# Kernel tuning notes

Measured on AMD Instinct MI355X. Metric: run time of the kernel, lower is better.

The kernel has to match this reference:

```python
import jax, jax.numpy as jnp
import numpy as np

DELTA = 0.1
NEG_INF = -1e30


def setup_inputs() -> dict:
    key = jax.random.key(0)
    k1, k2, k3, k4 = jax.random.split(key, 4)
    Bs, Bt, D, C = 8192, 8192, 64, 10
    return {
        "src_feas": jax.random.normal(k1, (Bs, D), dtype=jnp.float32),
        "src_labels": jax.random.randint(k2, (Bs,), 0, C, dtype=jnp.int32),
        "tgt_feas": jax.random.normal(k3, (Bt, D), dtype=jnp.float32),
        "tgt_logits": jax.random.normal(k4, (Bt, C), dtype=jnp.float32),
    }


def reference(src_feas, src_labels, tgt_feas, tgt_logits):
    # The original builds the explicit list of positive pairs (i_tgt, j_src)
    # where tgt sample i is 'confident' (top1-top2 logit gap >= delta) and
    # src_labels[j] == argmax(tgt_logits[i]).  The [P, P] score matrix it
    # forms is s[k, l] = src_feas[j_k] . tgt_feas[i_l], which only depends on
    # (j_k, i_l), so sum(diag(log_softmax(s))) collapses to a weighted
    # logsumexp over the [Bs, Bt] cross-domain score matrix. Same math,
    # fully vectorized, order-invariant.
    Bs = src_feas.shape[0]
    C = tgt_logits.shape[1]

    top2 = jax.lax.top_k(tgt_logits, 2)[0]                  # [Bt, 2]
    conf = (top2[:, 0] - top2[:, 1]) >= DELTA               # [Bt]
    cls = jnp.argmax(tgt_logits, axis=1)                    # [Bt]

    # per-class count of source samples
    counts = jnp.zeros((C,), jnp.float32).at[src_labels].add(1.0)  # [C]
    # w[i] = multiplicity of tgt sample i in the pair list
    w = jnp.where(conf, counts[cls], 0.0)                   # [Bt]

    M = src_feas @ tgt_feas.T                               # [Bs, Bt]
    logw = jnp.where(w > 0, jnp.log(jnp.maximum(w, 1.0)), NEG_INF)
    # L[j] = log sum over all pairs l of exp(M[j, i_l])
    L = jax.scipy.special.logsumexp(M + logw[None, :], axis=1)  # [Bs]

    pair_mask = conf[None, :] & (src_labels[:, None] == cls[None, :])  # [Bs, Bt]
    nce_sum = jnp.sum(jnp.where(pair_mask, M - L[:, None], 0.0))
    P = jnp.sum(w)                                          # total pair count
    nce = nce_sum / (-1.0 * Bs * P)
    return nce
```

## Files before the change

### kernel.cpp

```cpp
#include <hip/hip_runtime.h>
#include <hip/hip_bf16.h>

#define BSZ 8192
#define BTZ 8192
#define DD 64
#define NC 10
#define SHIFT2 20.0f
#define LN2 0.69314718055994531f
#define LOG2E 1.44269504088896341f

typedef __attribute__((ext_vector_type(8))) short bf16x8;
typedef __attribute__((ext_vector_type(4))) float f32x4;

#if defined(__has_builtin)
#if __has_builtin(__builtin_amdgcn_exp2f)
#define EXP2(x) __builtin_amdgcn_exp2f(x)
#else
#define EXP2(x) exp2f(x)
#endif
#else
#define EXP2(x) exp2f(x)
#endif

__device__ __forceinline__ unsigned short f2bf_rne(float f) {
    unsigned int u = __float_as_uint(f);
    u += 0x7FFFu + ((u >> 16) & 1u);
    return (unsigned short)(u >> 16);
}

__global__ __launch_bounds__(256) void kAB(
    const float4* __restrict__ src4, const float4* __restrict__ tgt4,
    const int* __restrict__ labels, const float* __restrict__ logits,
    ushort4* __restrict__ srcb, ushort4* __restrict__ tgtb,
    float* __restrict__ S, float* __restrict__ counts,
    float* __restrict__ cc_part, unsigned char* __restrict__ cls8,
    float* __restrict__ colbias)
{
    int t = threadIdx.x;
    if (blockIdx.x < 512) {
        int tid = blockIdx.x * 256 + t;
        float4 s = src4[tid];
        ushort4 os;
        os.x = f2bf_rne(s.x * LOG2E); os.y = f2bf_rne(s.y * LOG2E);
        os.z = f2bf_rne(s.z * LOG2E); os.w = f2bf_rne(s.w * LOG2E);
        srcb[tid] = os;
        float4 v = tgt4[tid];
        ushort4 ot; ot.x = f2bf_rne(v.x); ot.y = f2bf_rne(v.y);
        ot.z = f2bf_rne(v.z); ot.w = f2bf_rne(v.w);
        tgtb[tid] = ot;
        return;
    }
    __shared__ float lcnt[NC];
    __shared__ float hist[NC];
    __shared__ float hred[4][NC];
    int b = blockIdx.x - 512;
    int i = b * 256 + t;
    int w = t >> 6, lane = t & 63;

    float c10[NC];
    #pragma unroll
    for (int c = 0; c < NC; ++c) c10[c] = 0.0f;
    for (int k = 0; k < 32; ++k) {
        int lab = labels[t + 256 * k];
        #pragma unroll
        for (int c = 0; c < NC; ++c) c10[c] += (lab == c) ? 1.0f : 0.0f;
    }
    #pragma unroll
    for (int c = 0; c < NC; ++c) {
        float v = c10[c];
        #pragma unroll
        for (int m = 1; m < 64; m <<= 1) v += __shfl_xor(v, m);
        if (lane == 0) hred[w][c] = v;
    }
    if (t < NC) hist[t] = 0.0f;
    __syncthreads();
    if (t < NC) lcnt[t] = hred[0][t] + hred[1][t] + hred[2][t] + hred[3][t];
    __syncthreads();
    if (b == 0 && t < NC) counts[t] = lcnt[t];

    float m1 = -3.0e38f, m2 = -3.0e38f; int cls = 0;
    #pragma unroll
    for (int c = 0; c < NC; ++c) {
        float v = logits[i * NC + c];
        if (v > m1) { m2 = m1; m1 = v; cls = c; }
        else if (v > m2) { m2 = v; }
    }
    bool conf = (m1 - m2) >= 0.1f;
    float cnt = lcnt[cls];
    bool live = conf && (cnt > 0.0f);
    colbias[i] = live ? (log2f(cnt) - SHIFT2) : -1.0e30f;
    cls8[i] = live ? (unsigned char)cls : (unsigned char)255;
    S[i] = 0.0f;
    if (conf) atomicAdd(&hist[cls], 1.0f);
    __syncthreads();
    if (t < NC) cc_part[b * NC + t] = hist[t];
}

__global__ __launch_bounds__(256, 4) void kC(
    const unsigned short* __restrict__ srcb, const unsigned short* __restrict__ tgtb,
    const float* __restrict__ colbias, float* __restrict__ S,
    const float* __restrict__ srcf, const float* __restrict__ tgtf,
    const int* __restrict__ labels, const unsigned char* __restrict__ cls8,
    float* __restrict__ SC, float* __restrict__ T)
{
    int t = threadIdx.x;
    if (blockIdx.x >= 4096) {
        int bb = blockIdx.x - 4096;
        bool isT = bb >= 32;
        int rb = (bb & 31) * 256;
        const float* F = isT ? tgtf : srcf;
        int w = t >> 6, lane = t & 63;
        float acc[NC];
        #pragma unroll
        for (int c = 0; c < NC; ++c) acc[c] = 0.0f;
        int row0 = rb + w * 64;
        for (int r = 0; r < 64; ++r) {
            int row = row0 + r;
            int lab = isT ? (int)cls8[row] : labels[row];
            float f = F[row * DD + lane];
            #pragma unroll
            for (int c = 0; c < NC; ++c) acc[c] += (lab == c) ? f : 0.0f;
        }
        float* OUT = isT ? T : SC;
        #pragma unroll
        for (int c = 0; c < NC; ++c) atomicAdd(&OUT[c * DD + lane], acc[c]);
        return;
    }

    __shared__ float lds[4][64];
    int w = t >> 6;
    int lane = t & 63;
    int l15 = lane & 15;
    int quad = lane >> 4;
    int colchunk = blockIdx.x & 31;
    int rowg = blockIdx.x >> 5;
    int row_base = rowg * 64;

    bf16x8 a[4][2];
    #pragma unroll
    for (int mb = 0; mb < 4; ++mb) {
        const bf16x8* p = (const bf16x8*)(srcb + (size_t)(row_base + mb * 16 + l15) * DD + quad * 8);
        a[mb][0] = p[0];
        a[mb][1] = p[4];
    }
    int col0 = colchunk * 256 + w * 64;
    bf16x8 b[4][2];
    float cb2[4];
    #pragma unroll
    for (int ct = 0; ct < 4; ++ct) {
        int cc = col0 + ct * 16 + l15;
        const bf16x8* q = (const bf16x8*)(tgtb + (size_t)cc * DD + quad * 8);
        b[ct][0] = q[0];
        b[ct][1] = q[4];
        cb2[ct] = colbias[cc];
    }

    float rs[4][4];
    #pragma unroll
    for (int mb = 0; mb < 4; ++mb)
        #pragma unroll
        for (int r = 0; r < 4; ++r) rs[mb][r] = 0.0f;

    #pragma unroll
    for (int ct = 0; ct < 4; ++ct) {
        #pragma unroll
        for (int mb = 0; mb < 4; ++mb) {
            f32x4 acc = {cb2[ct], cb2[ct], cb2[ct], cb2[ct]};
            acc = __builtin_amdgcn_mfma_f32_16x16x32_bf16(a[mb][0], b[ct][0], acc, 0, 0, 0);
            acc = __builtin_amdgcn_mfma_f32_16x16x32_bf16(a[mb][1], b[ct][1], acc, 0, 0, 0);
            #pragma unroll
            for (int r = 0; r < 4; ++r)
                rs[mb][r] += EXP2(acc[r]);
        }
    }

    #pragma unroll
    for (int mb = 0; mb < 4; ++mb) {
        #pragma unroll
        for (int r = 0; r < 4; ++r) {
            float v = rs[mb][r];
            v += __shfl_xor(v, 1);
            v += __shfl_xor(v, 2);
            v += __shfl_xor(v, 4);
            v += __shfl_xor(v, 8);
            if (l15 == 0) lds[w][mb * 16 + quad * 4 + r] = v;
        }
    }
    __syncthreads();
    if (t < 64)
        atomicAdd(&S[row_base + t], lds[0][t] + lds[1][t] + lds[2][t] + lds[3][t]);
}

__global__ __launch_bounds__(256) void kD(
    const float* __restrict__ S, const int* __restrict__ labels,
    const float* __restrict__ counts, const float* __restrict__ cc_part,
    const float* __restrict__ SC, const float* __restrict__ T,
    float* __restrict__ gACC, int* __restrict__ gcnt,
    float* __restrict__ out)
{
    __shared__ float cc[NC];
    __shared__ float redL[4], red1[4], redP[4];
    __shared__ int isLast;
    int t = threadIdx.x;
    int w = t >> 6, lane = t & 63;
    if (t < NC) {
        float s = 0.0f;
        #pragma unroll
        for (int k = 0; k < 32; ++k) s += cc_part[k * NC + t];
        cc[t] = s;
    }
    __syncthreads();
    int j = blockIdx.x * 256 + t;
    float L = (log2f(S[j]) + SHIFT2) * LN2;
    float tl = cc[labels[j]] * L;
    #pragma unroll
    for (int m = 1; m < 64; m <<= 1) tl += __shfl_xor(tl, m);
    if (lane == 0) redL[w] = tl;
    __syncthreads();
    if (t == 0) {
        float v = redL[0] + redL[1] + redL[2] + redL[3];
        atomicAdd(&gACC[0], v);
        __threadfence();
        int old = atomicAdd(gcnt, 1);
        isLast = (old == 31) ? 1 : 0;
    }
    __syncthreads();
    if (!isLast) return;

    float t1 = 0.0f;
    for (int o = t; o < NC * DD; o += 256) t1 += SC[o] * T[o];
    float Pp = (t < NC) ? counts[t] * cc[t] : 0.0f;
    #pragma unroll
    for (int m = 1; m < 64; m <<= 1) {
        t1 += __shfl_xor(t1, m);
        Pp += __shfl_xor(Pp, m);
    }
    if (lane == 0) { red1[w] = t1; redP[w] = Pp; }
    __syncthreads();
    if (t == 0) {
        float term1 = red1[0] + red1[1] + red1[2] + red1[3];
        float P = redP[0] + redP[1] + redP[2] + redP[3];
        float termL = atomicAdd(&gACC[0], 0.0f);
        out[0] = (term1 - termL) / (-(float)BSZ * P);
    }
}

extern "C" void kernel_launch(void* const* d_in, const int* in_sizes, int n_in,
                              void* d_out, int out_size, void* d_ws, size_t ws_size,
                              hipStream_t stream) {
    const float* src    = (const float*)d_in[0];
    const int*   labels = (const int*)d_in[1];
    const float* tgt    = (const float*)d_in[2];
    const float* logits = (const float*)d_in[3];

    char* ws = (char*)d_ws;
    float* S        = (float*)(ws + 0);
    int*   gcnt     = (int*)(ws + 32768);
    float* gACC     = (float*)(ws + 32776);
    float* counts   = (float*)(ws + 32784);
    float* cc_part  = (float*)(ws + 32832);
    float* SC       = (float*)(ws + 34112);
    float* T        = (float*)(ws + 36672);
    float* colbias  = (float*)(ws + 40960);
    unsigned char* cls8 = (unsigned char*)(ws + 73728);
    unsigned short* srcb = (unsigned short*)(ws + 81920);
    unsigned short* tgtb = (unsigned short*)(ws + 81920 + 1048576);

    hipMemsetAsync(ws + 32768, 0, 8192, stream);
    kAB<<<544, 256, 0, stream>>>((const float4*)src, (const float4*)tgt, labels,
                                 logits, (ushort4*)srcb, (ushort4*)tgtb,
                                 S, counts, cc_part, cls8, colbias);
    kC<<<4160, 256, 0, stream>>>(srcb, tgtb, colbias, S,
                                 src, tgt, labels, cls8, SC, T);
    kD<<<32, 256, 0, stream>>>(S, labels, counts, cc_part, SC, T,
                               gACC, gcnt, (float*)d_out);
}
```

Baseline: 123.9 us.

## Fuse pair-score sum into MFMA tile loop and reuse target fragments across row groups

Removes the separate per-class feature-sum blocks (SC/T atomics) and instead accumulates the matched-pair score term directly from the MFMA outputs using label/class comparisons. Each kC block now keeps its target B fragments and column biases in registers and loops over four 64-row source groups, cutting the grid from 4160 to 1024 blocks and reloading B four times less often. Per-block partial term1 values are written out and reduced in kD, and the memset shrinks. The trade-off is extra compare/select ALU work per MFMA output, fewer blocks for latency hiding, and bf16-precision pair scores replacing the fp32 feature-sum dot product.

```diff
diff --git a/kernel.cpp b/kernel.cpp
--- a/kernel.cpp
+++ b/kernel.cpp
@@ -98,108 +98,109 @@
 
 __global__ __launch_bounds__(256, 4) void kC(
     const unsigned short* __restrict__ srcb, const unsigned short* __restrict__ tgtb,
-    const float* __restrict__ colbias, float* __restrict__ S,
-    const float* __restrict__ srcf, const float* __restrict__ tgtf,
-    const int* __restrict__ labels, const unsigned char* __restrict__ cls8,
-    float* __restrict__ SC, float* __restrict__ T)
+    const float* __restrict__ colbias, const unsigned char* __restrict__ cls8,
+    const int* __restrict__ labels,
+    float* __restrict__ S, float* __restrict__ term1_part)
 {
+    __shared__ float lds[4][64];
+    __shared__ float t1red[4];
     int t = threadIdx.x;
-    if (blockIdx.x >= 4096) {
-        int bb = blockIdx.x - 4096;
-        bool isT = bb >= 32;
-        int rb = (bb & 31) * 256;
-        const float* F = isT ? tgtf : srcf;
-        int w = t >> 6, lane = t & 63;
-        float acc[NC];
-        #pragma unroll
-        for (int c = 0; c < NC; ++c) acc[c] = 0.0f;
-        int row0 = rb + w * 64;
-        for (int r = 0; r < 64; ++r) {
-            int row = row0 + r;
-            int lab = isT ? (int)cls8[row] : labels[row];
-            float f = F[row * DD + lane];
-            #pragma unroll
-            for (int c = 0; c < NC; ++c) acc[c] += (lab == c) ? f : 0.0f;
-        }
-        float* OUT = isT ? T : SC;
-        #pragma unroll
-        for (int c = 0; c < NC; ++c) atomicAdd(&OUT[c * DD + lane], acc[c]);
-        return;
-    }
-
-    __shared__ float lds[4][64];
     int w = t >> 6;
     int lane = t & 63;
     int l15 = lane & 15;
     int quad = lane >> 4;
     int colchunk = blockIdx.x & 31;
-    int rowg = blockIdx.x >> 5;
-    int row_base = rowg * 64;
-
-    bf16x8 a[4][2];
-    #pragma unroll
-    for (int mb = 0; mb < 4; ++mb) {
-        const bf16x8* p = (const bf16x8*)(srcb + (size_t)(row_base + mb * 16 + l15) * DD + quad * 8);
-        a[mb][0] = p[0];
-        a[mb][1] = p[4];
-    }
+    int rowg0 = (blockIdx.x >> 5) << 2;
+
     int col0 = colchunk * 256 + w * 64;
-    bf16x8 b[4][2];
+    bf16x8 bfr[4][2];
     float cb2[4];
+    int ccls[4];
     #pragma unroll
     for (int ct = 0; ct < 4; ++ct) {
         int cc = col0 + ct * 16 + l15;
         const bf16x8* q = (const bf16x8*)(tgtb + (size_t)cc * DD + quad * 8);
-        b[ct][0] = q[0];
-        b[ct][1] = q[4];
+        bfr[ct][0] = q[0];
+        bfr[ct][1] = q[4];
         cb2[ct] = colbias[cc];
-    }
-
-    float rs[4][4];
-    #pragma unroll
-    for (int mb = 0; mb < 4; ++mb)
-        #pragma unroll
-        for (int r = 0; r < 4; ++r) rs[mb][r] = 0.0f;
-
-    #pragma unroll
-    for (int ct = 0; ct < 4; ++ct) {
+        ccls[ct] = (int)cls8[cc];
+    }
+
+    float t1p = 0.0f;
+    for (int it = 0; it < 4; ++it) {
+        int row_base = (rowg0 + it) * 64;
+
+        bf16x8 a[4][2];
+        int4 rl4[4];
         #pragma unroll
         for (int mb = 0; mb < 4; ++mb) {
-            f32x4 acc = {cb2[ct], cb2[ct], cb2[ct], cb2[ct]};
-            acc = __builtin_amdgcn_mfma_f32_16x16x32_bf16(a[mb][0], b[ct][0], acc, 0, 0, 0);
-            acc = __builtin_amdgcn_mfma_f32_16x16x32_bf16(a[mb][1], b[ct][1], acc, 0, 0, 0);
+            const bf16x8* p = (const bf16x8*)(srcb + (size_t)(row_base + mb * 16 + l15) * DD + quad * 8);
+            a[mb][0] = p[0];
+            a[mb][1] = p[4];
+            rl4[mb] = ((const int4*)labels)[(row_base + mb * 16 + quad * 4) >> 2];
+        }
+
+        float rs[4][4];
+        #pragma unroll
+        for (int mb = 0; mb < 4; ++mb)
             #pragma unroll
-            for (int r = 0; r < 4; ++r)
-                rs[mb][r] += EXP2(acc[r]);
+            for (int r = 0; r < 4; ++r) rs[mb][r] = 0.0f;
+
+        #pragma unroll
+        for (int ct = 0; ct < 4; ++ct) {
+            #pragma unroll
+            for (int mb = 0; mb < 4; ++mb) {
+                f32x4 acc = {cb2[ct], cb2[ct], cb2[ct], cb2[ct]};
+                acc = __builtin_amdgcn_mfma_f32_16x16x32_bf16(a[mb][0], bfr[ct][0], acc, 0, 0, 0);
+                acc = __builtin_amdgcn_mfma_f32_16x16x32_bf16(a[mb][1], bfr[ct][1], acc, 0, 0, 0);
+                int rl0 = rl4[mb].x, rl1 = rl4[mb].y, rl2 = rl4[mb].z, rl3 = rl4[mb].w;
+                float e0 = acc[0], e1 = acc[1], e2 = acc[2], e3 = acc[3];
+                rs[mb][0] += EXP2(e0);
+                rs[mb][1] += EXP2(e1);
+                rs[mb][2] += EXP2(e2);
+                rs[mb][3] += EXP2(e3);
+                t1p += (ccls[ct] == rl0) ? (e0 - cb2[ct]) : 0.0f;
+                t1p += (ccls[ct] == rl1) ? (e1 - cb2[ct]) : 0.0f;
+                t1p += (ccls[ct] == rl2) ? (e2 - cb2[ct]) : 0.0f;
+                t1p += (ccls[ct] == rl3) ? (e3 - cb2[ct]) : 0.0f;
+            }
         }
-    }
-
-    #pragma unroll
-    for (int mb = 0; mb < 4; ++mb) {
-        #pragma unroll
-        for (int r = 0; r < 4; ++r) {
-            float v = rs[mb][r];
-            v += __shfl_xor(v, 1);
-            v += __shfl_xor(v, 2);
-            v += __shfl_xor(v, 4);
-            v += __shfl_xor(v, 8);
-            if (l15 == 0) lds[w][mb * 16 + quad * 4 + r] = v;
+
+        #pragma unroll
+        for (int mb = 0; mb < 4; ++mb) {
+            #pragma unroll
+            for (int r = 0; r < 4; ++r) {
+                float v = rs[mb][r];
+                v += __shfl_xor(v, 1);
+                v += __shfl_xor(v, 2);
+                v += __shfl_xor(v, 4);
+                v += __shfl_xor(v, 8);
+                if (l15 == 0) lds[w][mb * 16 + quad * 4 + r] = v;
+            }
         }
-    }
-    __syncthreads();
-    if (t < 64)
-        atomicAdd(&S[row_base + t], lds[0][t] + lds[1][t] + lds[2][t] + lds[3][t]);
+        __syncthreads();
+        if (t < 64)
+            atomicAdd(&S[row_base + t], lds[0][t] + lds[1][t] + lds[2][t] + lds[3][t]);
+        __syncthreads();
+    }
+
+    #pragma unroll
+    for (int m = 1; m < 64; m <<= 1) t1p += __shfl_xor(t1p, m);
+    if (lane == 0) t1red[w] = t1p;
+    __syncthreads();
+    if (t == 0)
+        term1_part[blockIdx.x] = t1red[0] + t1red[1] + t1red[2] + t1red[3];
 }
 
 __global__ __launch_bounds__(256) void kD(
     const float* __restrict__ S, const int* __restrict__ labels,
     const float* __restrict__ counts, const float* __restrict__ cc_part,
-    const float* __restrict__ SC, const float* __restrict__ T,
+    const float* __restrict__ term1_part,
     float* __restrict__ gACC, int* __restrict__ gcnt,
     float* __restrict__ out)
 {
     __shared__ float cc[NC];
-    __shared__ float redL[4], red1[4], redP[4];
+    __shared__ float red[4], redP[4];
     __shared__ int isLast;
     int t = threadIdx.x;
     int w = t >> 6, lane = t & 63;
@@ -212,14 +213,14 @@
     __syncthreads();
     int j = blockIdx.x * 256 + t;
     float L = (log2f(S[j]) + SHIFT2) * LN2;
-    float tl = cc[labels[j]] * L;
-    #pragma unroll
-    for (int m = 1; m < 64; m <<= 1) tl += __shfl_xor(tl, m);
-    if (lane == 0) redL[w] = tl;
+    float v = -cc[labels[j]] * L;
+    if (t < 32) v += term1_part[blockIdx.x * 32 + t] * LN2;
+    #pragma unroll
+    for (int m = 1; m < 64; m <<= 1) v += __shfl_xor(v, m);
+    if (lane == 0) red[w] = v;
     __syncthreads();
     if (t == 0) {
-        float v = redL[0] + redL[1] + redL[2] + redL[3];
-        atomicAdd(&gACC[0], v);
+        atomicAdd(&gACC[0], red[0] + red[1] + red[2] + red[3]);
         __threadfence();
         int old = atomicAdd(gcnt, 1);
         isLast = (old == 31) ? 1 : 0;
@@ -227,21 +228,15 @@
     __syncthreads();
     if (!isLast) return;
 
-    float t1 = 0.0f;
-    for (int o = t; o < NC * DD; o += 256) t1 += SC[o] * T[o];
     float Pp = (t < NC) ? counts[t] * cc[t] : 0.0f;
     #pragma unroll
-    for (int m = 1; m < 64; m <<= 1) {
-        t1 += __shfl_xor(t1, m);
-        Pp += __shfl_xor(Pp, m);
-    }
-    if (lane == 0) { red1[w] = t1; redP[w] = Pp; }
+    for (int m = 1; m < 64; m <<= 1) Pp += __shfl_xor(Pp, m);
+    if (lane == 0) redP[w] = Pp;
     __syncthreads();
     if (t == 0) {
-        float term1 = red1[0] + red1[1] + red1[2] + red1[3];
         float P = redP[0] + redP[1] + redP[2] + redP[3];
-        float termL = atomicAdd(&gACC[0], 0.0f);
-        out[0] = (term1 - termL) / (-(float)BSZ * P);
+        float num = atomicAdd(&gACC[0], 0.0f);
+        out[0] = num / (-(float)BSZ * P);
     }
 }
 
@@ -254,24 +249,22 @@
     const float* logits = (const float*)d_in[3];
 
     char* ws = (char*)d_ws;
-    float* S        = (float*)(ws + 0);
-    int*   gcnt     = (int*)(ws + 32768);
-    float* gACC     = (float*)(ws + 32776);
-    float* counts   = (float*)(ws + 32784);
-    float* cc_part  = (float*)(ws + 32832);
-    float* SC       = (float*)(ws + 34112);
-    float* T        = (float*)(ws + 36672);
-    float* colbias  = (float*)(ws + 40960);
+    float* S          = (float*)(ws + 0);
+    int*   gcnt       = (int*)(ws + 32768);
+    float* gACC       = (float*)(ws + 32776);
+    float* counts     = (float*)(ws + 32832);
+    float* cc_part    = (float*)(ws + 32896);
+    float* term1_part = (float*)(ws + 34176);
+    float* colbias    = (float*)(ws + 40960);
     unsigned char* cls8 = (unsigned char*)(ws + 73728);
     unsigned short* srcb = (unsigned short*)(ws + 81920);
     unsigned short* tgtb = (unsigned short*)(ws + 81920 + 1048576);
 
-    hipMemsetAsync(ws + 32768, 0, 8192, stream);
+    hipMemsetAsync(ws + 32768, 0, 64, stream);
     kAB<<<544, 256, 0, stream>>>((const float4*)src, (const float4*)tgt, labels,
                                  logits, (ushort4*)srcb, (ushort4*)tgtb,
                                  S, counts, cc_part, cls8, colbias);
-    kC<<<4160, 256, 0, stream>>>(srcb, tgtb, colbias, S,
-                                 src, tgt, labels, cls8, SC, T);
-    kD<<<32, 256, 0, stream>>>(S, labels, counts, cc_part, SC, T,
+    kC<<<1024, 256, 0, stream>>>(srcb, tgtb, colbias, cls8, labels, S, term1_part);
+    kD<<<32, 256, 0, stream>>>(S, labels, counts, cc_part, term1_part,
                                gACC, gcnt, (float*)d_out);
 }
```

Result: slower. 139.8 us (+12.9%).
